# Performance work log

Measured on AMD Instinct MI355X. Metric: run time of the kernel, lower is better.

## Reference

```python
import jax, jax.numpy as jnp
import numpy as np

B, T, C = 2, 2048, 2048
H, D = 16, 128  # num_heads, head_dim


def setup_inputs() -> dict:
    key = jax.random.key(0)
    ks = jax.random.split(key, 5)
    x = jax.random.normal(ks[0], (B, T, C), dtype=jnp.float32)
    # causal mask: mask==0 positions are filled with -inf
    mask = jnp.tril(jnp.ones((T, T), dtype=jnp.int32))[None, None, :, :]
    wq = jax.random.normal(ks[1], (C, C), dtype=jnp.float32) * (C ** -0.5)
    wk = jax.random.normal(ks[2], (C, C), dtype=jnp.float32) * (C ** -0.5)
    wv = jax.random.normal(ks[3], (C, C), dtype=jnp.float32) * (C ** -0.5)
    wo = jax.random.normal(ks[4], (C, C), dtype=jnp.float32) * (C ** -0.5)
    return {"x": x, "mask": mask, "wq": wq, "wk": wk, "wv": wv, "wo": wo}


def reference(x, mask, wq, wk, wv, wo):
    Bx, Tx, Cx = x.shape
    scale = D ** -0.5
    # torch Linear: y = x @ W.T (weights are [out, in])
    q = (x @ wq.T).reshape(Bx, Tx, H, D).transpose(0, 2, 1, 3)  # [B,H,T,D]
    k = (x @ wk.T).reshape(Bx, Tx, H, D).transpose(0, 2, 1, 3)
    v = (x @ wv.T).reshape(Bx, Tx, H, D).transpose(0, 2, 1, 3)
    scores = jnp.einsum("bhqd,bhkd->bhqk", q, k) * scale  # [B,H,T,T]
    scores = jnp.where(mask == 0, -jnp.inf, scores)
    attn = jax.nn.softmax(scores, axis=-1)
    out = jnp.einsum("bhqk,bhkd->bhqd", attn, v)  # [B,H,T,D]
    out = out.transpose(0, 2, 1, 3).reshape(Bx, Tx, Cx)
    return out @ wo.T
```

## Files before the change

kernel.cpp:

```cpp
#include <hip/hip_runtime.h>
#include <hip/hip_bf16.h>


#define BB 2
#define TT 2048
#define CC 2048
#define HH 16
#define DD 128
#define MM (BB*TT)
#define NQT (TT/64)
#define GNT (CC/64)

typedef __bf16 bf16x8 __attribute__((ext_vector_type(8)));
typedef __bf16 bf16x4 __attribute__((ext_vector_type(4)));
typedef float  f32x4  __attribute__((ext_vector_type(4)));

#define MFMA16(a, b, c) __builtin_amdgcn_mfma_f32_16x16x32_bf16((a), (b), (c), 0, 0, 0)

__device__ __forceinline__ void g2lds16(const void* g, void* l) {
    __builtin_amdgcn_global_load_lds(
        (const __attribute__((address_space(1))) void*)g,
        (__attribute__((address_space(3))) void*)l,
        16, 0, 0);
}

__global__ __launch_bounds__(256) void cvt_f32_bf16(
    const float* __restrict__ in, __bf16* __restrict__ out, int n4)
{
    const int i = blockIdx.x * 256 + threadIdx.x;
    if (i < n4) {
        const float4 v = ((const float4*)in)[i];
        bf16x4 o;
        o.x = (__bf16)v.x; o.y = (__bf16)v.y;
        o.z = (__bf16)v.z; o.w = (__bf16)v.w;
        ((bf16x4*)out)[i] = o;
    }
}

__global__ __launch_bounds__(256) void cvt4_f32_bf16(
    const float* __restrict__ w0, const float* __restrict__ w1,
    const float* __restrict__ w2, const float* __restrict__ w3,
    __bf16* __restrict__ o0, __bf16* __restrict__ o1,
    __bf16* __restrict__ o2, __bf16* __restrict__ o3)
{
    const float* in; __bf16* out;
    switch (blockIdx.y) {
        case 0:  in = w0; out = o0; break;
        case 1:  in = w1; out = o1; break;
        case 2:  in = w2; out = o2; break;
        default: in = w3; out = o3; break;
    }
    const int i = blockIdx.x * 256 + threadIdx.x;
    const float4 v = ((const float4*)in)[i];
    bf16x4 o;
    o.x = (__bf16)v.x; o.y = (__bf16)v.y;
    o.z = (__bf16)v.z; o.w = (__bf16)v.w;
    ((bf16x4*)out)[i] = o;
}

template<int MODE>
__global__ __launch_bounds__(512, 2) void gemm_bt(
    const __bf16* __restrict__ A, const __bf16* __restrict__ Wt,
    void* __restrict__ out)
{
    __shared__ __align__(16) __bf16 As[3][256*64];
    __shared__ __align__(16) __bf16 Bs[3][2][128*32];

    const int tid = threadIdx.x;
    const int w   = tid >> 6, lane = tid & 63;
    const int wm  = w >> 1,  wn  = w & 1;
    const int lo  = lane & 15, hi = lane >> 4;
    const int xr  = (lo & 7) << 4;
    const int xb2 = ((lo >> 1) & 3) << 4;

    const int bid   = blockIdx.y * gridDim.x + blockIdx.x;
    const int xcd   = bid & 7, loc = bid >> 3;
    const int n0    = (2*xcd + (loc & 1)) * 128;
    const int m0    = (loc >> 1) * 256;

    const int ar   = tid >> 3, as_ = tid & 7;
    const int acol = ((as_ ^ (ar & 7)) << 3);
    const int br   = tid >> 2, bs_ = tid & 3;
    const int bcol = ((bs_ ^ ((br >> 1) & 3)) << 3);

    auto stageA3a = [&](int buf, int kt) {
        #pragma unroll
        for (int j = 0; j < 3; ++j)
            g2lds16(A + (size_t)(m0 + j*64 + ar)*CC + kt*64 + acol,
                    (char*)&As[buf][0] + j*8192 + w*1024);
    };
    auto stageA3b = [&](int buf, int kt) {
        g2lds16(A + (size_t)(m0 + 3*64 + ar)*CC + kt*64 + acol,
                (char*)&As[buf][0] + 3*8192 + w*1024);
        #pragma unroll
        for (int kh = 0; kh < 2; ++kh)
            g2lds16(Wt + (size_t)(n0 + br)*CC + kt*64 + kh*32 + bcol,
                    (char*)&Bs[buf][kh][0] + w*1024);
    };
    auto rdA = [&](bf16x8* af, int buf, int ks) {
        const char* base = (const char*)&As[buf][0];
        #pragma unroll
        for (int mf = 0; mf < 4; ++mf) {
            const int r = wm*64 + mf*16 + lo;
            af[mf] = *(const bf16x8*)(base + r*128 + ((ks*64 + hi*16) ^ xr));
        }
    };
    auto rdB = [&](bf16x8* bv, int buf, int ks) {
        const char* base = (const char*)&Bs[buf][ks][0];
        #pragma unroll
        for (int nf = 0; nf < 4; ++nf) {
            const int n = wn*64 + nf*16 + lo;
            bv[nf] = *(const bf16x8*)(base + n*64 + ((hi*16) ^ xb2));
        }
    };

    f32x4 acc[4][4] = {};

    stageA3a(0, 0); stageA3b(0, 0);
    stageA3a(1, 1); stageA3b(1, 1);
    asm volatile("s_waitcnt vmcnt(6)" ::: "memory");
    __builtin_amdgcn_s_barrier();

    int rb = 0;
    #pragma unroll 1
    for (int t = 0; t < GNT - 2; ++t) {
        const int sb = (rb == 0) ? 2 : rb - 1;
        {
            bf16x8 af[4], bv[4];
            rdA(af, rb, 0); rdB(bv, rb, 0);
            stageA3a(sb, t + 2);
            __builtin_amdgcn_s_barrier();
            __builtin_amdgcn_s_setprio(1);
            #pragma unroll
            for (int mf = 0; mf < 4; ++mf)
                #pragma unroll
                for (int nf = 0; nf < 4; ++nf)
                    acc[mf][nf] = MFMA16(af[mf], bv[nf], acc[mf][nf]);
            __builtin_amdgcn_s_setprio(0);
            __builtin_amdgcn_s_barrier();
        }
        {
            bf16x8 af[4], bv[4];
            rdA(af, rb, 1); rdB(bv, rb, 1);
            stageA3b(sb, t + 2);
            __builtin_amdgcn_s_barrier();
            __builtin_amdgcn_s_setprio(1);
            #pragma unroll
            for (int mf = 0; mf < 4; ++mf)
                #pragma unroll
                for (int nf = 0; nf < 4; ++nf)
                    acc[mf][nf] = MFMA16(af[mf], bv[nf], acc[mf][nf]);
            __builtin_amdgcn_s_setprio(0);
            asm volatile("s_waitcnt vmcnt(6)" ::: "memory");
            __builtin_amdgcn_s_barrier();
        }
        rb = (rb == 2) ? 0 : rb + 1;
    }
    {
        bf16x8 af[4], bv[4];
        rdA(af, rb, 0); rdB(bv, rb, 0);
        __builtin_amdgcn_s_barrier();
        #pragma unroll
        for (int mf = 0; mf < 4; ++mf)
            #pragma unroll
            for (int nf = 0; nf < 4; ++nf)
                acc[mf][nf] = MFMA16(af[mf], bv[nf], acc[mf][nf]);
        __builtin_amdgcn_s_barrier();
        rdA(af, rb, 1); rdB(bv, rb, 1);
        #pragma unroll
        for (int mf = 0; mf < 4; ++mf)
            #pragma unroll
            for (int nf = 0; nf < 4; ++nf)
                acc[mf][nf] = MFMA16(af[mf], bv[nf], acc[mf][nf]);
        asm volatile("s_waitcnt vmcnt(0)" ::: "memory");
        __builtin_amdgcn_s_barrier();
        rb = (rb == 2) ? 0 : rb + 1;
    }
    {
        bf16x8 af[4], bv[4];
        rdA(af, rb, 0); rdB(bv, rb, 0);
        #pragma unroll
        for (int mf = 0; mf < 4; ++mf)
            #pragma unroll
            for (int nf = 0; nf < 4; ++nf)
                acc[mf][nf] = MFMA16(af[mf], bv[nf], acc[mf][nf]);
        rdA(af, rb, 1); rdB(bv, rb, 1);
        #pragma unroll
        for (int mf = 0; mf < 4; ++mf)
            #pragma unroll
            for (int nf = 0; nf < 4; ++nf)
                acc[mf][nf] = MFMA16(af[mf], bv[nf], acc[mf][nf]);
    }

    #pragma unroll
    for (int mf = 0; mf < 4; ++mf) {
        #pragma unroll
        for (int nf = 0; nf < 4; ++nf) {
            #pragma unroll
            for (int r = 0; r < 4; ++r) {
                const int row = m0 + wm*64 + mf*16 + hi*4 + r;
                const int col = n0 + wn*64 + nf*16 + lo;
                const float v = acc[mf][nf][r];
                if (MODE == 0) {
                    const int b = row >> 11, t = row & (TT-1);
                    const int h = col >> 7,  d = col & (DD-1);
                    ((__bf16*)out)[(size_t)((b*HH + h)*TT + t)*DD + d] = (__bf16)v;
                } else if (MODE == 1) {
                    const int b = row >> 11, t = row & (TT-1);
                    const int h = col >> 7,  d = col & (DD-1);
                    ((__bf16*)out)[(size_t)((b*HH + h)*DD + d)*TT + t] = (__bf16)v;
                } else {
                    ((float*)out)[(size_t)row*CC + col] = v;
                }
            }
        }
    }
}

__global__ __launch_bounds__(256, 2) void attn_fwd(
    const __bf16* __restrict__ Q, const __bf16* __restrict__ K,
    const __bf16* __restrict__ Vt, __bf16* __restrict__ O)
{
    __shared__ __align__(16) __bf16 Ks[2][64*128];
    __shared__ __align__(16) __bf16 Vs[2][128*64];
    __shared__ __align__(16) __bf16 Ps[4][16*64];

    const int bh  = blockIdx.y;
    const int tid = threadIdx.x;
    const int w   = tid >> 6, lane = tid & 63;
    const int lo  = lane & 15, hi = lane >> 4;
    const int xr  = (lo & 7) << 4;

    const int krow_l  = lane >> 4;
    const int kcol_sw = ((lane & 15) << 4);
    const int vrow_l  = lane >> 3;
    const int vcol_sw = (((lane & 7) ^ (lane >> 3)) << 3);

    const size_t kbase = (size_t)bh * TT * DD;
    const size_t vbase = (size_t)bh * DD * TT;
    const int b = bh >> 4, h = bh & 15;

    auto stage = [&](int buf, int kv0) {
        #pragma unroll
        for (int i = 0; i < 4; ++i) {
            const int c = 4*w + i;
            {
                const int row = 4*c + krow_l;
                const int sw  = (kcol_sw ^ ((row & 7) << 4)) >> 1;
                g2lds16(K + kbase + (size_t)(kv0 + row)*DD + sw,
                        &Ks[buf][0] + c*512);
            }
            {
                const int row = 8*c + vrow_l;
                g2lds16(Vt + vbase + (size_t)row*TT + kv0 + vcol_sw,
                        &Vs[buf][0] + c*512);
            }
        }
    };

    #pragma unroll 1
    for (int half = 0; half < 2; ++half) {
        const int qt = half ? (int)blockIdx.x : (NQT - 1 - (int)blockIdx.x);
        const int q0 = qt * 64;

        const __bf16* Qbase = Q + (kbase + (size_t)(q0 + w*16 + lo) * DD);
        bf16x8 qf[4];
        #pragma unroll
        for (int kc = 0; kc < 4; ++kc)
            qf[kc] = *(const bf16x8*)(Qbase + kc*32 + hi*8);

        float mrow[4], lrow[4];
        #pragma unroll
        for (int r = 0; r < 4; ++r) { mrow[r] = -1e30f; lrow[r] = 0.f; }
        f32x4 oacc[8] = {};

        const int qg_base = q0 + w*16 + hi*4;
        const int ntiles  = qt + 1;

        stage(0, 0);
        __syncthreads();
        int cur = 0;

        for (int t = 0; t < ntiles; ++t) {
            const int kv0 = t*64;
            if (t + 1 < ntiles) stage(cur ^ 1, (t+1)*64);

            const char* Kb = (const char*)&Ks[cur][0];
            const char* Vb = (const char*)&Vs[cur][0];

            f32x4 s[4];
            __builtin_amdgcn_s_setprio(1);
            #pragma unroll
            for (int st = 0; st < 4; ++st) {
                f32x4 a = {};
                #pragma unroll
                for (int kc = 0; kc < 4; ++kc) {
                    const bf16x8 kf = *(const bf16x8*)(
                        Kb + (st*16 + lo)*256 + ((kc*64 + hi*16) ^ xr));
                    a = MFMA16(qf[kc], kf, a);
                }
                s[st] = a;
            }
            __builtin_amdgcn_s_setprio(0);

            float pmax[4];
            const bool diag = (t == ntiles - 1);
            #pragma unroll
            for (int r = 0; r < 4; ++r) {
                const int qg = qg_base + r;
                float mx = -1e30f;
                #pragma unroll
                for (int st = 0; st < 4; ++st) {
                    float v = s[st][r] * 0.08838834764831845f;
                    if (diag) {
                        const int kvg = kv0 + st*16 + lo;
                        v = (kvg > qg) ? -1e30f : v;
                    }
                    s[st][r] = v;
                    mx = fmaxf(mx, v);
                }
                #pragma unroll
                for (int msk = 1; msk < 16; msk <<= 1)
                    mx = fmaxf(mx, __shfl_xor(mx, msk, 64));
                pmax[r] = mx;
            }

            float rsc[4], psum[4];
            #pragma unroll
            for (int r = 0; r < 4; ++r) {
                const float mnew = fmaxf(mrow[r], pmax[r]);
                rsc[r]  = __expf(mrow[r] - mnew);
                mrow[r] = mnew;
                float ps = 0.f;
                #pragma unroll
                for (int st = 0; st < 4; ++st) {
                    const float pv = __expf(s[st][r] - mnew);
                    s[st][r] = pv;
                    ps += pv;
                }
                psum[r] = ps;
            }
            #pragma unroll
            for (int r = 0; r < 4; ++r) {
                #pragma unroll
                for (int msk = 1; msk < 16; msk <<= 1)
                    psum[r] += __shfl_xor(psum[r], msk, 64);
                lrow[r] = lrow[r]*rsc[r] + psum[r];
            }
            #pragma unroll
            for (int dc = 0; dc < 8; ++dc)
                #pragma unroll
                for (int r = 0; r < 4; ++r)
                    oacc[dc][r] *= rsc[r];

            char* Pw = (char*)&Ps[w][0];
            #pragma unroll
            for (int st = 0; st < 4; ++st)
                #pragma unroll
                for (int r = 0; r < 4; ++r) {
                    const int row = hi*4 + r;
                    *(__bf16*)(Pw + row*128 + (((st*16 + lo)*2) ^ ((row & 7) << 4)))
                        = (__bf16)s[st][r];
                }

            __builtin_amdgcn_s_setprio(1);
            #pragma unroll
            for (int kc2 = 0; kc2 < 2; ++kc2) {
                const bf16x8 pf = *(const bf16x8*)(
                    Pw + lo*128 + ((kc2*64 + hi*16) ^ xr));
                #pragma unroll
                for (int dc = 0; dc < 8; ++dc) {
                    const bf16x8 vf = *(const bf16x8*)(
                        Vb + (dc*16 + lo)*128 + ((kc2*64 + hi*16) ^ xr));
                    oacc[dc] = MFMA16(pf, vf, oacc[dc]);
                }
            }
            __builtin_amdgcn_s_setprio(0);

            __syncthreads();
            cur ^= 1;
        }

        #pragma unroll
        for (int r = 0; r < 4; ++r) {
            const float inv = 1.f / lrow[r];
            const int qg = qg_base + r;
            #pragma unroll
            for (int dc = 0; dc < 8; ++dc) {
                const int d = dc*16 + lo;
                O[(size_t)(b*TT + qg)*CC + h*DD + d] = (__bf16)(oacc[dc][r] * inv);
            }
        }
    }
}

extern "C" void kernel_launch(void* const* d_in, const int* in_sizes, int n_in,
                              void* d_out, int out_size, void* d_ws, size_t ws_size,
                              hipStream_t stream) {
    const float* x  = (const float*)d_in[0];
    const float* wq = (const float*)d_in[2];
    const float* wk = (const float*)d_in[3];
    const float* wv = (const float*)d_in[4];
    const float* wo = (const float*)d_in[5];

    char* p = (char*)d_ws;
    __bf16* xb  = (__bf16*)p; p += (size_t)MM*CC*2;
    __bf16* wqb = (__bf16*)p; p += (size_t)CC*CC*2;
    __bf16* wkb = (__bf16*)p; p += (size_t)CC*CC*2;
    __bf16* wvb = (__bf16*)p; p += (size_t)CC*CC*2;
    __bf16* wob = (__bf16*)p; p += (size_t)CC*CC*2;
    __bf16* Qb  = (__bf16*)p; p += (size_t)MM*CC*2;
    __bf16* Kb  = (__bf16*)p; p += (size_t)MM*CC*2;
    __bf16* Vtb = (__bf16*)p; p += (size_t)MM*CC*2;
    __bf16* AOb = xb;

    cvt_f32_bf16<<<MM*CC/4/256, 256, 0, stream>>>(x, xb, MM*CC/4);
    cvt4_f32_bf16<<<dim3(CC*CC/4/256, 4), 256, 0, stream>>>(
        wq, wk, wv, wo, wqb, wkb, wvb, wob);

    const dim3 gg(CC/128, MM/256);
    gemm_bt<0><<<gg, 512, 0, stream>>>(xb, wqb, Qb);
    gemm_bt<0><<<gg, 512, 0, stream>>>(xb, wkb, Kb);
    gemm_bt<1><<<gg, 512, 0, stream>>>(xb, wvb, Vtb);

    attn_fwd<<<dim3(NQT/2, BB*HH), 256, 0, stream>>>(Qb, Kb, Vtb, AOb);

    gemm_bt<2><<<gg, 512, 0, stream>>>(AOb, wob, (void*)d_out);
}
```

Before: 255.9 us.

## Fuse conversions and QKV GEMMs, add lazy softmax rescale with exp2

The five fp32-to-bf16 conversion launches are merged into one kernel over a contiguous workspace. The three Q/K/V projection GEMMs become a single launch over a concatenated 6144-wide weight, with per-segment output layouts and a new tile mapping. In attention, the log2(e) factor is folded into the score scale so exp2 can be used, and the running-max rescale of the output accumulator is skipped unless the max grows past a threshold. Attention block indexing is also remapped so consecutive blocks cover different heads. The workspace layout must be contiguous for the fused paths to work, and the lazy rescale relies on fp32 headroom.

```diff
diff --git a/kernel.cpp b/kernel.cpp
--- a/kernel.cpp
+++ b/kernel.cpp
@@ -24,38 +24,25 @@
         16, 0, 0);
 }
 
-__global__ __launch_bounds__(256) void cvt_f32_bf16(
-    const float* __restrict__ in, __bf16* __restrict__ out, int n4)
+__global__ __launch_bounds__(256) void cvt_all(
+    const float* __restrict__ x,  const float* __restrict__ wq,
+    const float* __restrict__ wk, const float* __restrict__ wv,
+    const float* __restrict__ wo, __bf16* __restrict__ out_base)
 {
-    const int i = blockIdx.x * 256 + threadIdx.x;
-    if (i < n4) {
-        const float4 v = ((const float4*)in)[i];
-        bf16x4 o;
-        o.x = (__bf16)v.x; o.y = (__bf16)v.y;
-        o.z = (__bf16)v.z; o.w = (__bf16)v.w;
-        ((bf16x4*)out)[i] = o;
-    }
-}
-
-__global__ __launch_bounds__(256) void cvt4_f32_bf16(
-    const float* __restrict__ w0, const float* __restrict__ w1,
-    const float* __restrict__ w2, const float* __restrict__ w3,
-    __bf16* __restrict__ o0, __bf16* __restrict__ o1,
-    __bf16* __restrict__ o2, __bf16* __restrict__ o3)
-{
-    const float* in; __bf16* out;
-    switch (blockIdx.y) {
-        case 0:  in = w0; out = o0; break;
-        case 1:  in = w1; out = o1; break;
-        case 2:  in = w2; out = o2; break;
-        default: in = w3; out = o3; break;
-    }
-    const int i = blockIdx.x * 256 + threadIdx.x;
-    const float4 v = ((const float4*)in)[i];
+    const int idx = blockIdx.x * 256 + threadIdx.x;
+    const float* in; int off;
+    if (idx < (1 << 21)) { in = x; off = idx; }
+    else {
+        const int r = idx - (1 << 21);
+        const int k = r >> 20;
+        in  = (k == 0) ? wq : (k == 1) ? wk : (k == 2) ? wv : wo;
+        off = r & ((1 << 20) - 1);
+    }
+    const float4 v = ((const float4*)in)[off];
     bf16x4 o;
     o.x = (__bf16)v.x; o.y = (__bf16)v.y;
     o.z = (__bf16)v.z; o.w = (__bf16)v.w;
-    ((bf16x4*)out)[i] = o;
+    ((bf16x4*)out_base)[idx] = o;
 }
 
 template<int MODE>
@@ -75,8 +62,9 @@
 
     const int bid   = blockIdx.y * gridDim.x + blockIdx.x;
     const int xcd   = bid & 7, loc = bid >> 3;
-    const int n0    = (2*xcd + (loc & 1)) * 128;
-    const int m0    = (loc >> 1) * 256;
+    int n0, m0;
+    if (MODE == 3) { n0 = (xcd*6 + (loc >> 4)) * 128; m0 = (loc & 15) * 256; }
+    else           { n0 = (2*xcd + (loc & 1)) * 128;  m0 = (loc >> 1) * 256; }
 
     const int ar   = tid >> 3, as_ = tid & 7;
     const int acol = ((as_ ^ (ar & 7)) << 3);
@@ -192,6 +180,7 @@
                 acc[mf][nf] = MFMA16(af[mf], bv[nf], acc[mf][nf]);
     }
 
+    const int seg = n0 >> 11;
     #pragma unroll
     for (int mf = 0; mf < 4; ++mf) {
         #pragma unroll
@@ -201,14 +190,15 @@
                 const int row = m0 + wm*64 + mf*16 + hi*4 + r;
                 const int col = n0 + wn*64 + nf*16 + lo;
                 const float v = acc[mf][nf][r];
-                if (MODE == 0) {
+                if (MODE == 3) {
+                    __bf16* dst = (__bf16*)out + (size_t)seg * MM * CC;
                     const int b = row >> 11, t = row & (TT-1);
-                    const int h = col >> 7,  d = col & (DD-1);
-                    ((__bf16*)out)[(size_t)((b*HH + h)*TT + t)*DD + d] = (__bf16)v;
-                } else if (MODE == 1) {
-                    const int b = row >> 11, t = row & (TT-1);
-                    const int h = col >> 7,  d = col & (DD-1);
-                    ((__bf16*)out)[(size_t)((b*HH + h)*DD + d)*TT + t] = (__bf16)v;
+                    const int c2 = col & (CC-1);
+                    const int h = c2 >> 7, d = c2 & (DD-1);
+                    if (seg < 2)
+                        dst[(size_t)((b*HH + h)*TT + t)*DD + d] = (__bf16)v;
+                    else
+                        dst[(size_t)((b*HH + h)*DD + d)*TT + t] = (__bf16)v;
                 } else {
                     ((float*)out)[(size_t)row*CC + col] = v;
                 }
@@ -225,7 +215,9 @@
     __shared__ __align__(16) __bf16 Vs[2][128*64];
     __shared__ __align__(16) __bf16 Ps[4][16*64];
 
-    const int bh  = blockIdx.y;
+    const int lid   = blockIdx.y * gridDim.x + blockIdx.x;
+    const int bh    = lid & 31;
+    const int pairx = lid >> 5;
     const int tid = threadIdx.x;
     const int w   = tid >> 6, lane = tid & 63;
     const int lo  = lane & 15, hi = lane >> 4;
@@ -239,6 +231,7 @@
     const size_t kbase = (size_t)bh * TT * DD;
     const size_t vbase = (size_t)bh * DD * TT;
     const int b = bh >> 4, h = bh & 15;
+    const float SC = 0.12754613142f;
 
     auto stage = [&](int buf, int kv0) {
         #pragma unroll
@@ -260,7 +253,7 @@
 
     #pragma unroll 1
     for (int half = 0; half < 2; ++half) {
-        const int qt = half ? (int)blockIdx.x : (NQT - 1 - (int)blockIdx.x);
+        const int qt = half ? pairx : (NQT - 1 - pairx);
         const int q0 = qt * 64;
 
         const __bf16* Qbase = Q + (kbase + (size_t)(q0 + w*16 + lo) * DD);
@@ -311,7 +304,7 @@
                 float mx = -1e30f;
                 #pragma unroll
                 for (int st = 0; st < 4; ++st) {
-                    float v = s[st][r] * 0.08838834764831845f;
+                    float v = s[st][r] * SC;
                     if (diag) {
                         const int kvg = kv0 + st*16 + lo;
                         v = (kvg > qg) ? -1e30f : v;
@@ -325,16 +318,33 @@
                 pmax[r] = mx;
             }
 
-            float rsc[4], psum[4];
+            bool need = false;
+            #pragma unroll
+            for (int r = 0; r < 4; ++r)
+                need = need || (pmax[r] > mrow[r] + 11.5f);
+            if (__any(need)) {
+                float rsc[4];
+                #pragma unroll
+                for (int r = 0; r < 4; ++r) {
+                    const float mnew = fmaxf(mrow[r], pmax[r]);
+                    rsc[r]  = __builtin_amdgcn_exp2f(mrow[r] - mnew);
+                    mrow[r] = mnew;
+                    lrow[r] *= rsc[r];
+                }
+                #pragma unroll
+                for (int dc = 0; dc < 8; ++dc)
+                    #pragma unroll
+                    for (int r = 0; r < 4; ++r)
+                        oacc[dc][r] *= rsc[r];
+            }
+
+            float psum[4];
             #pragma unroll
             for (int r = 0; r < 4; ++r) {
-                const float mnew = fmaxf(mrow[r], pmax[r]);
-                rsc[r]  = __expf(mrow[r] - mnew);
-                mrow[r] = mnew;
                 float ps = 0.f;
                 #pragma unroll
                 for (int st = 0; st < 4; ++st) {
-                    const float pv = __expf(s[st][r] - mnew);
+                    const float pv = __builtin_amdgcn_exp2f(s[st][r] - mrow[r]);
                     s[st][r] = pv;
                     ps += pv;
                 }
@@ -345,13 +355,8 @@
                 #pragma unroll
                 for (int msk = 1; msk < 16; msk <<= 1)
                     psum[r] += __shfl_xor(psum[r], msk, 64);
-                lrow[r] = lrow[r]*rsc[r] + psum[r];
-            }
-            #pragma unroll
-            for (int dc = 0; dc < 8; ++dc)
-                #pragma unroll
-                for (int r = 0; r < 4; ++r)
-                    oacc[dc][r] *= rsc[r];
+                lrow[r] += psum[r];
+            }
 
             char* Pw = (char*)&Ps[w][0];
             #pragma unroll
@@ -413,17 +418,13 @@
     __bf16* Kb  = (__bf16*)p; p += (size_t)MM*CC*2;
     __bf16* Vtb = (__bf16*)p; p += (size_t)MM*CC*2;
     __bf16* AOb = xb;
-
-    cvt_f32_bf16<<<MM*CC/4/256, 256, 0, stream>>>(x, xb, MM*CC/4);
-    cvt4_f32_bf16<<<dim3(CC*CC/4/256, 4), 256, 0, stream>>>(
-        wq, wk, wv, wo, wqb, wkb, wvb, wob);
-
-    const dim3 gg(CC/128, MM/256);
-    gemm_bt<0><<<gg, 512, 0, stream>>>(xb, wqb, Qb);
-    gemm_bt<0><<<gg, 512, 0, stream>>>(xb, wkb, Kb);
-    gemm_bt<1><<<gg, 512, 0, stream>>>(xb, wvb, Vtb);
+    (void)wkb; (void)wvb;
+
+    cvt_all<<<24576, 256, 0, stream>>>(x, wq, wk, wv, wo, xb);
+
+    gemm_bt<3><<<dim3(48, 16), 512, 0, stream>>>(xb, wqb, (void*)Qb);
 
     attn_fwd<<<dim3(NQT/2, BB*HH), 256, 0, stream>>>(Qb, Kb, Vtb, AOb);
 
-    gemm_bt<2><<<gg, 512, 0, stream>>>(AOb, wob, (void*)d_out);
+    gemm_bt<2><<<dim3(16, 16), 512, 0, stream>>>(AOb, wob, (void*)d_out);
 }
```

Measured after the change: 279.2 us. 9.1% more time.
